# Performance work log

Hardware: AMD Instinct MI355X
Metric: run time of the kernel (lower is better)

The kernel has to match this reference:

```python
import jax, jax.numpy as jnp
import numpy as np

N, E = 50000, 250000
SD, VM = 128, 64          # scalar channels, vector multiplicity (irreps: 128x0e + 64x1e)
EA, SH = 64, 4            # edge_attr dim, spherical-harmonics dim (1x0e + 1x1e)
H, FC = 16, 256
HD = FC // H              # head dim = 16
EPS = 1e-5


def _split(x):
    return x[:, :SD], x[:, SD:].reshape(-1, VM, 3)


def _ln(s, V):
    # equivariant layer norm: standardize scalars; RMS-normalize vector norms
    s = (s - s.mean(-1, keepdims=True)) * jax.lax.rsqrt(s.var(-1, keepdims=True) + EPS)
    vn = jax.lax.rsqrt(jnp.mean(jnp.sum(V * V, -1), -1, keepdims=True) + EPS)
    return s, V * vn[..., None]


def setup_inputs() -> dict:
    key = jax.random.key(0)
    ks = iter(jax.random.split(key, 48))
    rn = lambda shp, sc=1.0: jax.random.normal(next(ks), shp, dtype=jnp.float32) * sc
    w = lambda i, o: rn((i, o), 1.0 / np.sqrt(i))
    z = lambda d: jnp.zeros((d,), jnp.float32)
    return dict(
        node_features=rn((N, SD + 3 * VM)),
        edge_attr=rn((E, EA)),
        edge_sh=rn((E, SH)),
        Wq=w(SD, FC), bq=z(FC),
        Wk=w(SD, FC), bk=z(FC),
        We=w(EA, FC), be=z(FC),
        Wv_s=w(SD, SD), bv_s=z(SD), Wv_v=w(VM, VM),
        w_ss=w(SD, SD), w_vv_s=w(VM, SD), w_ssg=w(SD, VM), w_vvg=w(VM, VM),
        b_ms=z(SD), b_mg=z(VM),
        w_sv=w(SD, VM), w_vs=w(VM, VM), w_vvv=w(VM, VM),
        Wo_s=w(SD, SD), bo_s=z(SD), Wo_v=w(VM, VM),
        W1_s=w(SD, SD + VM), b1_s=z(SD + VM), W1_v=w(VM, VM),
        W2_s=w(SD, SD), b2_s=z(SD), W2_v=w(VM, VM),
        edge_index=jax.random.randint(next(ks), (2, E), 0, N, dtype=jnp.int32),
        batch=jnp.zeros((N,), jnp.int32),
    )


def reference(node_features, edge_attr, edge_sh, Wq, bq, Wk, bk, We, be,
              Wv_s, bv_s, Wv_v, w_ss, w_vv_s, w_ssg, w_vvg, b_ms, b_mg,
              w_sv, w_vs, w_vvv, Wo_s, bo_s, Wo_v,
              W1_s, b1_s, W1_v, W2_s, b2_s, W2_v, edge_index, batch):
    src, dst = edge_index[0], edge_index[1]
    ns, nV = _split(node_features)                        # [N,SD], [N,VM,3]

    # per-edge multi-head attention scores (gathered q/k + edge bias term)
    q = (ns[dst] @ Wq + bq).reshape(-1, H, HD)
    k = (ns[src] @ Wk + bk).reshape(-1, H, HD)
    ef = (edge_attr @ We + be).reshape(-1, H, HD)
    scores = ((q * k).sum(-1) + (q * ef).sum(-1)) / np.sqrt(HD)   # [E,H]

    # per-destination-node softmax (replaces the python unique(dst) loop)
    m = jax.ops.segment_max(scores, dst, num_segments=N)
    ex = jnp.exp(scores - m[dst])
    den = jax.ops.segment_sum(ex, dst, num_segments=N)
    attn = (ex / den[dst]).mean(-1, keepdims=True)                # [E,1]

    # v projection (o3.Linear) on source nodes
    vs = ns[src] @ Wv_s + bv_s                                    # [E,SD]
    Vv = jnp.einsum('evk,vu->euk', nV[src], Wv_v)                 # [E,VM,3]

    # message MLP: fully-connected tensor product with edge SH, norm, swish-gate
    shs, shv = edge_sh[:, 0], edge_sh[:, 1:4]
    s_in = vs * shs[:, None]                                      # 0e x 0e -> 0e
    dots = jnp.einsum('evk,ek->ev', Vv, shv)                      # 1e x 1e -> 0e
    ms = s_in @ w_ss + dots @ w_vv_s + b_ms                       # [E,SD] scalars
    mg = s_in @ w_ssg + dots @ w_vvg + b_mg                       # [E,VM] gates
    MV = ((vs @ w_sv)[:, :, None] * shv[:, None, :]               # 0e x 1e -> 1e
          + jnp.einsum('evk,vu->euk', Vv * shs[:, None, None], w_vs)   # 1e x 0e -> 1e
          + jnp.einsum('evk,vu->euk', jnp.cross(Vv, shv[:, None, :]), w_vvv))  # 1e x 1e -> 1e
    sg, MVn = _ln(jnp.concatenate([ms, mg], -1), MV)
    msg_s = jax.nn.silu(sg[:, :SD])
    msg_V = MVn * jax.nn.sigmoid(sg[:, SD:])[:, :, None]

    # attention-weighted scatter-sum aggregation to destination nodes
    agg_s = jax.ops.segment_sum(msg_s * attn, dst, num_segments=N)
    agg_V = jax.ops.segment_sum(msg_V * attn[:, :, None], dst, num_segments=N)

    # out projection + residual + norm1
    x_s = ns + (agg_s @ Wo_s + bo_s)
    x_V = nV + jnp.einsum('nvk,vu->nuk', agg_V, Wo_v)
    x_s, x_V = _ln(x_s, x_V)

    # gated equivariant FFN + residual + norm2
    f = x_s @ W1_s + b1_s                                         # [N,SD+VM]
    fV = jnp.einsum('nvk,vu->nuk', x_V, W1_v)
    gV = fV * jax.nn.sigmoid(f[:, SD:])[:, :, None]
    o_s = x_s + (jax.nn.silu(f[:, :SD]) @ W2_s + b2_s)
    o_V = x_V + jnp.einsum('nvk,vu->nuk', gV, W2_v)
    o_s, o_V = _ln(o_s, o_V)
    return jnp.concatenate([o_s, o_V.reshape(-1, 3 * VM)], -1)
```

## Files before the change

### kernel.cpp

```cpp
#include <hip/hip_runtime.h>
#include <hip/hip_bf16.h>

#define NNODE 50000
#define NEDGE 250000

typedef __hip_bfloat16 bf16;
typedef __attribute__((ext_vector_type(8))) short short8v;
typedef __attribute__((ext_vector_type(4))) float f32x4;

__device__ __forceinline__ float b2f(bf16 x){ return __bfloat162float(x); }
__device__ __forceinline__ bf16  f2b(float x){ return __float2bfloat16(x); }
__device__ __forceinline__ short f2s(float x){ bf16 h=f2b(x); short s; __builtin_memcpy(&s,&h,2); return s; }
__device__ __forceinline__ float s2f(short s){ bf16 h; __builtin_memcpy(&h,&s,2); return b2f(h); }
__device__ __forceinline__ float sigm(float x){ return 1.0f/(1.0f+__expf(-x)); }
__device__ __forceinline__ float wred64(float v){
  #pragma unroll
  for(int o=32;o>0;o>>=1) v+=__shfl_xor(v,o,64);
  return v;
}
__device__ __forceinline__ float gred16(float v){
  v+=__shfl_xor(v,1,64); v+=__shfl_xor(v,2,64); v+=__shfl_xor(v,4,64); v+=__shfl_xor(v,8,64);
  return v;
}
__device__ __forceinline__ int ired64(int v){
  #pragma unroll
  for(int o=32;o>0;o>>=1) v+=__shfl_xor(v,o,64);
  return v;
}
__device__ __forceinline__ int fragOff(int r, int k){
  int kt=k>>5, k32=k&31, half=k32>>4, g=(k32&15)>>2, j=k32&3;
  return (kt<<10)+((r+(g<<4))<<4)+(half<<3)+(j<<1);
}
__device__ __forceinline__ short8v pack8(float4 a, float4 b){
  short8v s; s[0]=f2s(a.x);s[1]=f2s(a.y);s[2]=f2s(a.z);s[3]=f2s(a.w);
  s[4]=f2s(b.x);s[5]=f2s(b.y);s[6]=f2s(b.z);s[7]=f2s(b.w); return s;
}
__device__ __forceinline__ short8v pack8s(short4 a, short4 b){
  short8v s; s[0]=a.x;s[1]=a.y;s[2]=a.z;s[3]=a.w;s[4]=b.x;s[5]=b.y;s[6]=b.z;s[7]=b.w; return s;
}

#define T_WOS 0
#define T_WOV 32
#define T_W1S 40
#define T_W1V 88
#define T_W2S 96
#define T_W2V 128
#define T_WE  136
#define T_WQ  168
#define T_WK  232
#define T_WVS 296
#define T_WSS 328
#define T_WSSG 360
#define T_WSV 376
#define T_WVV 392
#define T_WVVS 400
#define T_WVVG 416
#define T_WVS2 424
#define T_WVVV 432
#define T_TOT 440

__global__ __launch_bounds__(64) void k_prep(
  const float* __restrict__ Wo_s, const float* __restrict__ Wo_v,
  const float* __restrict__ W1_s, const float* __restrict__ W1_v,
  const float* __restrict__ W2_s, const float* __restrict__ W2_v,
  const float* __restrict__ WeM,
  const float* __restrict__ Wq, const float* __restrict__ Wk,
  const float* __restrict__ Wv_s,
  const float* __restrict__ w_ss, const float* __restrict__ w_ssg,
  const float* __restrict__ w_sv,
  const float* __restrict__ Wv_v, const float* __restrict__ w_vv_s,
  const float* __restrict__ w_vvg, const float* __restrict__ w_vs,
  const float* __restrict__ w_vvv,
  short* __restrict__ P)
{
  const int T=blockIdx.x, l=threadIdx.x;
  const float* W; int N, KT, lt;
  if(T<T_WOV){ W=Wo_s; N=128; KT=4; lt=T; }
  else if(T<T_W1S){ W=Wo_v; N=64; KT=2; lt=T-T_WOV; }
  else if(T<T_W1V){ W=W1_s; N=192; KT=4; lt=T-T_W1S; }
  else if(T<T_W2S){ W=W1_v; N=64; KT=2; lt=T-T_W1V; }
  else if(T<T_W2V){ W=W2_s; N=128; KT=4; lt=T-T_W2S; }
  else if(T<T_WE){ W=W2_v; N=64; KT=2; lt=T-T_W2V; }
  else if(T<T_WQ){ W=WeM; N=256; KT=2; lt=T-T_WE; }
  else if(T<T_WK){ W=Wq; N=256; KT=4; lt=T-T_WQ; }
  else if(T<T_WVS){ W=Wk; N=256; KT=4; lt=T-T_WK; }
  else if(T<T_WSS){ W=Wv_s; N=128; KT=4; lt=T-T_WVS; }
  else if(T<T_WSSG){ W=w_ss; N=128; KT=4; lt=T-T_WSS; }
  else if(T<T_WSV){ W=w_ssg; N=64; KT=4; lt=T-T_WSSG; }
  else if(T<T_WVV){ W=w_sv; N=64; KT=4; lt=T-T_WSV; }
  else if(T<T_WVVS){ W=Wv_v; N=64; KT=2; lt=T-T_WVV; }
  else if(T<T_WVVG){ W=w_vv_s; N=128; KT=2; lt=T-T_WVVS; }
  else if(T<T_WVS2){ W=w_vvg; N=64; KT=2; lt=T-T_WVVG; }
  else if(T<T_WVVV){ W=w_vs; N=64; KT=2; lt=T-T_WVS2; }
  else { W=w_vvv; N=64; KT=2; lt=T-T_WVVV; }
  const int nt=lt/KT, kt=lt-nt*KT;
  const int col=nt*16+(l&15);
  short8v o;
  #pragma unroll
  for(int j=0;j<8;j++){
    int k=kt*32+((j>>2)<<4)+((l>>4)<<2)+(j&3);
    o[j]=f2s(W[(size_t)k*N+col]);
  }
  *(short8v*)(P+((size_t)T<<9)+(l<<3))=o;
}


__global__ __launch_bounds__(256) void k1_mfma(
  const float* __restrict__ nf, const short* __restrict__ P,
  const float* __restrict__ bq, const float* __restrict__ bk,
  const float* __restrict__ bvs,
  bf16* __restrict__ Q, bf16* __restrict__ K, short* __restrict__ NREC2)
{
  __shared__ __align__(16) short nsF[4*512];
  __shared__ __align__(16) short vsF[4*512];
  const int t=threadIdx.x, l=t&63, w=t>>6;
  const int n0=blockIdx.x*16;
  for(int i=t;i<512;i+=256){
    int r=i>>5, c=(i&31)<<2;
    const float4 v=*(const float4*)&nf[(size_t)(n0+r)*320+c];
    short4 s; s.x=f2s(v.x); s.y=f2s(v.y); s.z=f2s(v.z); s.w=f2s(v.w);
    *(short4*)((char*)nsF+fragOff(r,c))=s;
  }
  __syncthreads();
  short8v a[4];
  #pragma unroll
  for(int kt=0;kt<4;kt++) a[kt]=*(const short8v*)((const char*)nsF+(kt<<10)+(l<<4));
  #pragma unroll
  for(int ii=0;ii<4;ii++){
    int nt=w+(ii<<2);
    f32x4 accq={0.f,0.f,0.f,0.f}, acck={0.f,0.f,0.f,0.f};
    #pragma unroll
    for(int kt=0;kt<4;kt++){
      short8v bq8=*(const short8v*)(P+(((size_t)(T_WQ+nt*4+kt))<<9)+(l<<3));
      short8v bk8=*(const short8v*)(P+(((size_t)(T_WK+nt*4+kt))<<9)+(l<<3));
      accq=__builtin_amdgcn_mfma_f32_16x16x32_bf16(a[kt],bq8,accq,0,0,0);
      acck=__builtin_amdgcn_mfma_f32_16x16x32_bf16(a[kt],bk8,acck,0,0,0);
    }
    int col=(nt<<4)+(l&15);
    float bqs=bq[col], bks=bk[col];
    #pragma unroll
    for(int r=0;r<4;r++){
      int row=((l>>4)<<2)+r;
      Q[(size_t)(n0+row)*256+col]=f2b(accq[r]+bqs);
      K[(size_t)(n0+row)*256+col]=f2b(acck[r]+bks);
    }
  }
  #pragma unroll
  for(int ii=0;ii<2;ii++){
    int nt=w+(ii<<2);
    f32x4 acc={0.f,0.f,0.f,0.f};
    #pragma unroll
    for(int kt=0;kt<4;kt++){
      short8v b=*(const short8v*)(P+(((size_t)(T_WVS+nt*4+kt))<<9)+(l<<3));
      acc=__builtin_amdgcn_mfma_f32_16x16x32_bf16(a[kt],b,acc,0,0,0);
    }
    int col=(nt<<4)+(l&15);
    float bv=bvs[col];
    #pragma unroll
    for(int r=0;r<4;r++){
      int row=((l>>4)<<2)+r;
      *(short*)((char*)vsF+fragOff(row,col))=f2s(acc[r]+bv);
    }
  }
  __syncthreads();
  #pragma unroll
  for(int kt=0;kt<4;kt++) a[kt]=*(const short8v*)((const char*)vsF+(kt<<10)+(l<<4));
  #pragma unroll
  for(int ii=0;ii<4;ii++){
    int nt=w+(ii<<2);
    int bt;
    if(nt<8) bt=T_WSS+nt*4;
    else if(nt<12) bt=T_WSSG+(nt-8)*4;
    else bt=T_WSV+(nt-12)*4;
    f32x4 acc={0.f,0.f,0.f,0.f};
    #pragma unroll
    for(int kt=0;kt<4;kt++){
      short8v b=*(const short8v*)(P+(((size_t)(bt+kt))<<9)+(l<<3));
      acc=__builtin_amdgcn_mfma_f32_16x16x32_bf16(a[kt],b,acc,0,0,0);
    }
    int col=(nt<<4)+(l&15);
    int lane, sslot;
    if(nt<8){ lane=col&63; sslot=(col>=64)?1:0; }
    else if(nt<12){ lane=col-128; sslot=2; }
    else { lane=col-192; sslot=3; }
    #pragma unroll
    for(int r=0;r<4;r++){
      int row=((l>>4)<<2)+r;
      NREC2[(size_t)(n0+row)*1280 + (lane<<2) + sslot]=f2s(acc[r]);
    }
  }
}

__global__ __launch_bounds__(256) void k2_mfma(
  const float* __restrict__ nf, const short* __restrict__ P,
  short* __restrict__ NREC2)
{
  __shared__ __align__(16) short nvF[6*512];
  __shared__ __align__(16) short vvF[6*512];
  const int t=threadIdx.x, l=t&63, w=t>>6;
  const int n0=blockIdx.x*16;
  for(int i=t;i<3072;i+=256){
    int r=i/192, c=i-r*192;
    int v=c/3, k=c-3*v;
    float x=nf[(size_t)(n0+r)*320+128+c];
    *(short*)((char*)nvF+(k<<11)+fragOff(r,v))=f2s(x);
  }
  __syncthreads();
  #pragma unroll
  for(int jj=0;jj<3;jj++){
    int job=w+(jj<<2);
    int p=job>>2, nt=job&3;
    f32x4 acc={0.f,0.f,0.f,0.f};
    #pragma unroll
    for(int kt=0;kt<2;kt++){
      short8v a2=*(const short8v*)((const char*)nvF+(p<<11)+(kt<<10)+(l<<4));
      short8v b=*(const short8v*)(P+(((size_t)(T_WVV+nt*2+kt))<<9)+(l<<3));
      acc=__builtin_amdgcn_mfma_f32_16x16x32_bf16(a2,b,acc,0,0,0);
    }
    int col=(nt<<4)+(l&15);
    #pragma unroll
    for(int r=0;r<4;r++){
      int row=((l>>4)<<2)+r;
      *(short*)((char*)vvF+(p<<11)+fragOff(row,col))=f2s(acc[r]);
    }
  }
  __syncthreads();
  #pragma unroll
  for(int jj=0;jj<15;jj++){
    int job=w+(jj<<2);
    int p=job/20, r20=job-p*20;
    int nt, bt, G0;
    if(r20<8){ nt=r20; bt=T_WVVS+nt*2; G0=0; }
    else if(r20<12){ nt=r20-8; bt=T_WVVG+nt*2; G0=1; }
    else if(r20<16){ nt=r20-12; bt=T_WVS2+nt*2; G0=2; }
    else { nt=r20-16; bt=T_WVVV+nt*2; G0=3; }
    f32x4 acc={0.f,0.f,0.f,0.f};
    #pragma unroll
    for(int kt=0;kt<2;kt++){
      short8v a2=*(const short8v*)((const char*)vvF+(p<<11)+(kt<<10)+(l<<4));
      short8v b=*(const short8v*)(P+(((size_t)(bt+kt))<<9)+(l<<3));
      acc=__builtin_amdgcn_mfma_f32_16x16x32_bf16(a2,b,acc,0,0,0);
    }
    int col=(nt<<4)+(l&15);
    int G;
    if(G0==0)      G = p*2 + (col>=64 ? 1 : 0);
    else if(G0==1) G = 6 + p;
    else if(G0==2) G = 9 + p;
    else           G = 12 + p;
    int lane = col & 63;
    int addr = ((1+(G>>2))<<8) + (lane<<2) + (G&3);
    #pragma unroll
    for(int r=0;r<4;r++){
      int row=((l>>4)<<2)+r;
      NREC2[(size_t)(n0+row)*1280 + addr]=f2s(acc[r]);
    }
  }
}

#define SCAN_NB 196

__global__ __launch_bounds__(256) void k_scan1(const int* __restrict__ counts, int* __restrict__ bsum){
  const int t=threadIdx.x, ln=t&63, wid=t>>6;
  int idx=blockIdx.x*256+t;
  int v=(idx<NNODE)?counts[idx]:0;
  int s=ired64(v);
  __shared__ int ws[4];
  if(ln==0) ws[wid]=s;
  __syncthreads();
  if(t==0) bsum[blockIdx.x]=ws[0]+ws[1]+ws[2]+ws[3];
}

__global__ __launch_bounds__(256) void k_scan2(const int* __restrict__ bsum, int* __restrict__ boff){
  const int t=threadIdx.x, ln=t&63, wid=t>>6;
  int v=(t<SCAN_NB)?bsum[t]:0;
  int incl=v;
  #pragma unroll
  for(int o=1;o<64;o<<=1){ int x=__shfl_up(incl,o,64); if(ln>=o) incl+=x; }
  __shared__ int wtot[4], wpre[4];
  if(ln==63) wtot[wid]=incl;
  __syncthreads();
  if(t==0){ int s=0; for(int k=0;k<4;k++){ wpre[k]=s; s+=wtot[k]; } }
  __syncthreads();
  if(t<SCAN_NB) boff[t]=wpre[wid]+incl-v;
}

__global__ __launch_bounds__(256) void k_scan3(const int* __restrict__ counts, const int* __restrict__ boff,
                                               int* __restrict__ off, int* __restrict__ cursor){
  const int t=threadIdx.x, ln=t&63, wid=t>>6;
  int idx=blockIdx.x*256+t;
  int v=(idx<NNODE)?counts[idx]:0;
  int incl=v;
  #pragma unroll
  for(int o=1;o<64;o<<=1){ int x=__shfl_up(incl,o,64); if(ln>=o) incl+=x; }
  __shared__ int wtot[4], wpre[4];
  if(ln==63) wtot[wid]=incl;
  __syncthreads();
  if(t==0){ int s=0; for(int k=0;k<4;k++){ wpre[k]=s; s+=wtot[k]; } }
  __syncthreads();
  int excl=boff[blockIdx.x]+wpre[wid]+incl-v;
  if(idx<NNODE){ off[idx]=excl; cursor[idx]=excl; }
  if(idx==NNODE) off[NNODE]=NEDGE;
  if(blockIdx.x==SCAN_NB-1 && t==255) off[NNODE]=NEDGE;
}

__global__ __launch_bounds__(256) void k_scatter(
  const int* __restrict__ eidx, const float* __restrict__ esh,
  int* __restrict__ cursor, int* __restrict__ eord,
  int* __restrict__ srcs, float* __restrict__ eshs)
{
  int e=blockIdx.x*256+threadIdx.x;
  if(e<NEDGE){
    int d=eidx[NEDGE+e];
    int pos=atomicAdd(&cursor[d],1);
    eord[pos]=e;
    srcs[pos]=eidx[e];
    *(float4*)&eshs[(size_t)pos*4]=*(const float4*)&esh[(size_t)e*4];
  }
}

__global__ __launch_bounds__(256) void k3_mfma(
  const float* __restrict__ eattr, const int* __restrict__ eidx,
  const short* __restrict__ P, const float* __restrict__ be,
  const bf16* __restrict__ Q, const bf16* __restrict__ K,
  float* __restrict__ SC, int* __restrict__ counts)
{
  __shared__ __align__(16) short aeF[2*512];
  __shared__ __align__(16) float ef[16][260];
  __shared__ int ssrc[16], sdst[16];
  const int t=threadIdx.x, l=t&63, w=t>>6;
  const int e0=blockIdx.x*16;
  if(t<16){
    ssrc[t]=eidx[e0+t];
    int d=eidx[NEDGE+e0+t];
    sdst[t]=d;
    atomicAdd(&counts[d],1);
  }
  {
    int r=t>>4, c4=(t&15)<<2;
    const float4 v=*(const float4*)&eattr[(size_t)(e0+r)*64+c4];
    short4 s; s.x=f2s(v.x); s.y=f2s(v.y); s.z=f2s(v.z); s.w=f2s(v.w);
    *(short4*)((char*)aeF+fragOff(r,c4))=s;
  }
  __syncthreads();
  {
    short8v a0=*(const short8v*)((const char*)aeF+(l<<4));
    short8v a1=*(const short8v*)((const char*)aeF+1024+(l<<4));
    #pragma unroll
    for(int ii=0;ii<4;ii++){
      int nt=w+(ii<<2);
      f32x4 acc={0.f,0.f,0.f,0.f};
      short8v b0=*(const short8v*)(P+(((size_t)(T_WE+nt*2+0))<<9)+(l<<3));
      short8v b1=*(const short8v*)(P+(((size_t)(T_WE+nt*2+1))<<9)+(l<<3));
      acc=__builtin_amdgcn_mfma_f32_16x16x32_bf16(a0,b0,acc,0,0,0);
      acc=__builtin_amdgcn_mfma_f32_16x16x32_bf16(a1,b1,acc,0,0,0);
      int col=(nt<<4)+(l&15);
      float bv=be[col];
      #pragma unroll
      for(int r=0;r<4;r++){ int row=((l>>4)<<2)+r; ef[row][col]=acc[r]+bv; }
    }
  }
  __syncthreads();
  {
    const int h=l&15, qt=l>>4;
    const int ch=h*16+(qt<<2);
    #pragma unroll
    for(int j=0;j<4;j++){
      int el=w*4+j;
      int s=ssrc[el], d=sdst[el];
      short4 qs=*(const short4*)((const short*)Q+(size_t)d*256+ch);
      short4 ks=*(const short4*)((const short*)K+(size_t)s*256+ch);
      const float4 e4=*(const float4*)&ef[el][ch];
      float p = s2f(qs.x)*(s2f(ks.x)+e4.x)
              + s2f(qs.y)*(s2f(ks.y)+e4.y)
              + s2f(qs.z)*(s2f(ks.z)+e4.z)
              + s2f(qs.w)*(s2f(ks.w)+e4.w);
      p += __shfl_xor(p,16,64);
      p += __shfl_xor(p,32,64);
      if(qt==0) SC[(size_t)(e0+el)*16+h]=p*0.25f;
    }
  }
}

__global__ __launch_bounds__(256) void k5_att(
  const float* __restrict__ SC, const int* __restrict__ OFF,
  const int* __restrict__ EORD, float* __restrict__ ATTs)
{
  const int l=threadIdx.x&63;
  const int n=blockIdx.x*4+(threadIdx.x>>6);
  const int beg=OFF[n], end=OFF[n+1];
  const int j=l>>4, h=l&15;
  float mh=-1e30f;
  for(int i=beg+j;i<end;i+=4) mh=fmaxf(mh, SC[(size_t)EORD[i]*16+h]);
  mh=fmaxf(mh,__shfl_xor(mh,16,64));
  mh=fmaxf(mh,__shfl_xor(mh,32,64));
  float dh=0.f;
  for(int i=beg+j;i<end;i+=4) dh+=__expf(SC[(size_t)EORD[i]*16+h]-mh);
  dh+=__shfl_xor(dh,16,64);
  dh+=__shfl_xor(dh,32,64);
  float rdh=(end>beg)?1.f/dh:0.f;
  for(int i0=beg;i0<end;i0+=4){
    int i=i0+j;
    float a=0.f; bool act=(i<end);
    if(act) a=__expf(SC[(size_t)EORD[i]*16+h]-mh)*rdh;
    a=gred16(a);
    if(h==0 && act) ATTs[i]=a*(1.f/16.f);
  }
}

__global__ __launch_bounds__(256) void k6_agg(
  const int* __restrict__ SRCs, const float* __restrict__ ESHs,
  const short* __restrict__ NREC2, const float* __restrict__ ATTs,
  const int* __restrict__ OFF,
  const float* __restrict__ b_ms, const float* __restrict__ b_mg,
  float* __restrict__ AGS, float* __restrict__ AGV)
{
  const int l = threadIdx.x & 63;
  const int n = blockIdx.x*4 + (threadIdx.x>>6);
  const int beg=OFF[n], end=OFF[n+1];
  const float bmsa=b_ms[l], bmsb=b_ms[64+l], bmgv=b_mg[l];

  float as0=0.f,as1=0.f,av0acc=0.f,av1acc=0.f,av2acc=0.f;
  for(int i=beg;i<end;i++){
    const int s=SRCs[i];
    const float att=ATTs[i];
    const float4 sh4=*(const float4*)&ESHs[(size_t)i*4];
    const float shs=sh4.x, sh0=sh4.y, sh1=sh4.z, sh2=sh4.w;

    const short* R = NREC2 + (size_t)s*1280 + (l<<2);
    const short4 q0=*(const short4*)(R);
    const short4 q1=*(const short4*)(R+256);
    const short4 q2=*(const short4*)(R+512);
    const short4 q3=*(const short4*)(R+768);
    const short4 q4=*(const short4*)(R+1024);

    float msa = shs*s2f(q0.x) + s2f(q1.x)*sh0 + s2f(q1.z)*sh1 + s2f(q2.x)*sh2 + bmsa;
    float msb = shs*s2f(q0.y) + s2f(q1.y)*sh0 + s2f(q1.w)*sh1 + s2f(q2.y)*sh2 + bmsb;
    float mgv = shs*s2f(q0.z) + s2f(q2.z)*sh0 + s2f(q2.w)*sh1 + s2f(q3.x)*sh2 + bmgv;

    float sum = wred64(msa+msb+mgv);
    float sq  = wred64(msa*msa+msb*msb+mgv*mgv);
    float mean = sum*(1.f/192.f);
    float var  = sq*(1.f/192.f) - mean*mean;
    float rs   = rsqrtf(var + 1e-5f);

    const float svv=s2f(q0.w);
    const float w0=s2f(q3.y), w1=s2f(q3.z), w2=s2f(q3.w);
    const float c0=s2f(q4.x), c1=s2f(q4.y), c2=s2f(q4.z);
    float cr0 = c1*sh2 - c2*sh1;
    float cr1 = c2*sh0 - c0*sh2;
    float cr2 = c0*sh1 - c1*sh0;
    float mv0 = svv*sh0 + shs*w0 + cr0;
    float mv1 = svv*sh1 + shs*w1 + cr1;
    float mv2 = svv*sh2 + shs*w2 + cr2;
    float vsq = wred64(mv0*mv0+mv1*mv1+mv2*mv2);
    float vn  = rsqrtf(vsq*(1.f/64.f) + 1e-5f);

    float sga=(msa-mean)*rs, sgb=(msb-mean)*rs, sgg=(mgv-mean)*rs;
    float wV = vn * sigm(sgg) * att;
    as0 += sga*sigm(sga)*att;
    as1 += sgb*sigm(sgb)*att;
    av0acc += mv0*wV;
    av1acc += mv1*wV;
    av2acc += mv2*wV;
  }
  AGS[(size_t)n*128+l]     =as0;
  AGS[(size_t)n*128+64+l]  =as1;
  AGV[(size_t)n*192+l]     =av0acc;
  AGV[(size_t)n*192+64+l]  =av1acc;
  AGV[(size_t)n*192+128+l] =av2acc;
}

__global__ __launch_bounds__(256) void k7_mfma(
  const float* __restrict__ nf,
  const float* __restrict__ AGS, const float* __restrict__ AGV,
  const short* __restrict__ P,
  const float* __restrict__ bo_s, const float* __restrict__ b1_s, const float* __restrict__ b2_s,
  float* __restrict__ out)
{
  __shared__ float xs[16][132];
  __shared__ float xv[16][196];
  __shared__ short ffh[16][204];
  __shared__ __align__(16) short asA[4*512];
  __shared__ __align__(16) short avA[6*512];
  __shared__ float smean[16], srs[16], svn[16];
  const int t=threadIdx.x, l=t&63, w=t>>6;
  const int n0=blockIdx.x*16;
  const int lam=t&63, kt4=t>>6;
  const int fr=lam&15, fg=lam>>4;

  for(int i=t;i<2048;i+=256){ int r=i>>7,c=i&127; xs[r][c]=nf[(size_t)(n0+r)*320+c]; }
  for(int i=t;i<3072;i+=256){ int r=i/192,cc=i-r*192; int k=cc>>6,u=cc&63; xv[r][cc]=nf[(size_t)(n0+r)*320+128+u*3+k]; }
  {
    const float* base=&AGS[(size_t)(n0+fr)*128 + (kt4<<5) + (fg<<2)];
    float4 va=*(const float4*)base, vb=*(const float4*)(base+16);
    *(short8v*)((char*)asA+(kt4<<10)+(lam<<4))=pack8(va,vb);
  }
  for(int i=t;i<384;i+=256){
    int seg=i>>6, lm=i&63, r=lm&15, g=lm>>4;
    int p=seg>>1, k2=seg&1;
    const float* base=&AGV[(size_t)(n0+r)*192 + (p<<6) + (k2<<5) + (g<<2)];
    float4 va=*(const float4*)base, vb=*(const float4*)(base+16);
    *(short8v*)((char*)avA+(seg<<10)+(lm<<4))=pack8(va,vb);
  }
  __syncthreads();

  {
    short8v a[4];
    #pragma unroll
    for(int kt=0;kt<4;kt++) a[kt]=*(const short8v*)((const char*)asA+(kt<<10)+(l<<4));
    #pragma unroll
    for(int ii=0;ii<2;ii++){
      int nt=w+(ii<<2);
      f32x4 acc={0.f,0.f,0.f,0.f};
      #pragma unroll
      for(int kt=0;kt<4;kt++){
        short8v b=*(const short8v*)(P+(((size_t)(T_WOS+nt*4+kt))<<9)+(l<<3));
        acc=__builtin_amdgcn_mfma_f32_16x16x32_bf16(a[kt],b,acc,0,0,0);
      }
      int col=(nt<<4)+(l&15);
      float bv=bo_s[col];
      #pragma unroll
      for(int r=0;r<4;r++){ int row=((l>>4)<<2)+r; xs[row][col]+=acc[r]+bv; }
    }
    #pragma unroll
    for(int ii=0;ii<3;ii++){
      int tid=w*3+ii, p=tid>>2, nt2=tid&3;
      f32x4 acc={0.f,0.f,0.f,0.f};
      #pragma unroll
      for(int kt=0;kt<2;kt++){
        short8v a2=*(const short8v*)((const char*)avA+(((p<<1)+kt)<<10)+(l<<4));
        short8v b=*(const short8v*)(P+(((size_t)(T_WOV+nt2*2+kt))<<9)+(l<<3));
        acc=__builtin_amdgcn_mfma_f32_16x16x32_bf16(a2,b,acc,0,0,0);
      }
      int col=(p<<6)+(nt2<<4)+(l&15);
      #pragma unroll
      for(int r=0;r<4;r++){ int row=((l>>4)<<2)+r; xv[row][col]+=acc[r]; }
    }
  }
  __syncthreads();

  {
    const int nn=t>>4, g=t&15;
    float sum=0,sq=0;
    #pragma unroll
    for(int j=0;j<8;j++){ float x=xs[nn][g+16*j]; sum+=x; sq+=x*x; }
    sum=gred16(sum); sq=gred16(sq);
    float mean=sum*(1.f/128.f);
    float var=sq*(1.f/128.f)-mean*mean;
    float vsq=0;
    #pragma unroll
    for(int j=0;j<12;j++){ float x=xv[nn][g+16*j]; vsq+=x*x; }
    vsq=gred16(vsq);
    if(g==0){ smean[nn]=mean; srs[nn]=rsqrtf(var+1e-5f); svn[nn]=rsqrtf(vsq*(1.f/64.f)+1e-5f); }
  }
  __syncthreads();

  for(int i=t;i<512;i+=256){
    int r=i>>5, c=(i&31)<<2;
    float m=smean[r], rs=srs[r];
    float4 v=*(float4*)&xs[r][c];
    v.x=(v.x-m)*rs; v.y=(v.y-m)*rs; v.z=(v.z-m)*rs; v.w=(v.w-m)*rs;
    *(float4*)&xs[r][c]=v;
  }
  for(int i=t;i<768;i+=256){
    int r=i/48, c=(i-r*48)<<2;
    float vn=svn[r];
    float4 v=*(float4*)&xv[r][c];
    v.x*=vn; v.y*=vn; v.z*=vn; v.w*=vn;
    *(float4*)&xv[r][c]=v;
  }
  __syncthreads();
  {
    float4 va=*(const float4*)&xs[fr][(kt4<<5)+(fg<<2)];
    float4 vb=*(const float4*)&xs[fr][(kt4<<5)+16+(fg<<2)];
    *(short8v*)((char*)asA+(kt4<<10)+(lam<<4))=pack8(va,vb);
  }
  for(int i=t;i<384;i+=256){
    int seg=i>>6, lm=i&63, r=lm&15, g=lm>>4;
    int p=seg>>1, k2=seg&1;
    float4 va=*(const float4*)&xv[r][(p<<6)+(k2<<5)+(g<<2)];
    float4 vb=*(const float4*)&xv[r][(p<<6)+(k2<<5)+16+(g<<2)];
    *(short8v*)((char*)avA+(seg<<10)+(lm<<4))=pack8(va,vb);
  }
  __syncthreads();

  {
    short8v a[4];
    #pragma unroll
    for(int kt=0;kt<4;kt++) a[kt]=*(const short8v*)((const char*)asA+(kt<<10)+(l<<4));
    #pragma unroll
    for(int ii=0;ii<3;ii++){
      int nt=w+(ii<<2);
      f32x4 acc={0.f,0.f,0.f,0.f};
      #pragma unroll
      for(int kt=0;kt<4;kt++){
        short8v b=*(const short8v*)(P+(((size_t)(T_W1S+nt*4+kt))<<9)+(l<<3));
        acc=__builtin_amdgcn_mfma_f32_16x16x32_bf16(a[kt],b,acc,0,0,0);
      }
      int col=(nt<<4)+(l&15);
      float bv=b1_s[col];
      #pragma unroll
      for(int r=0;r<4;r++){ int row=((l>>4)<<2)+r; ffh[row][col]=f2s(acc[r]+bv); }
    }
  }
  __syncthreads();

  f32x4 g4acc[3];
  {
    #pragma unroll
    for(int ii=0;ii<3;ii++){
      int tid=w*3+ii, p=tid>>2, nt2=tid&3;
      f32x4 acc={0.f,0.f,0.f,0.f};
      #pragma unroll
      for(int kt=0;kt<2;kt++){
        short8v a2=*(const short8v*)((const char*)avA+(((p<<1)+kt)<<10)+(l<<4));
        short8v b=*(const short8v*)(P+(((size_t)(T_W1V+nt2*2+kt))<<9)+(l<<3));
        acc=__builtin_amdgcn_mfma_f32_16x16x32_bf16(a2,b,acc,0,0,0);
      }
      g4acc[ii]=acc;
    }
    for(int i=t;i<512;i+=256){
      int r=i>>5, c=(i&31)<<2;
      short4 sv4=*(short4*)&ffh[r][c];
      float x0=s2f(sv4.x), x1=s2f(sv4.y), x2=s2f(sv4.z), x3=s2f(sv4.w);
      sv4.x=f2s(x0*sigm(x0)); sv4.y=f2s(x1*sigm(x1)); sv4.z=f2s(x2*sigm(x2)); sv4.w=f2s(x3*sigm(x3));
      *(short4*)&ffh[r][c]=sv4;
    }
  }
  __syncthreads();

  {
    short4 sa=*(const short4*)&ffh[fr][(kt4<<5)+(fg<<2)];
    short4 sb=*(const short4*)&ffh[fr][(kt4<<5)+16+(fg<<2)];
    *(short8v*)((char*)asA+(kt4<<10)+(lam<<4))=pack8s(sa,sb);
  }
  {
    #pragma unroll
    for(int ii=0;ii<3;ii++){
      int tid=w*3+ii, nt2=tid&3;
      int uu=(nt2<<4)+(l&15);
      #pragma unroll
      for(int r=0;r<4;r++){
        int row=((l>>4)<<2)+r;
        g4acc[ii][r]*=sigm(s2f(ffh[row][128+uu]));
      }
    }
  }
  __syncthreads();

  {
    #pragma unroll
    for(int ii=0;ii<3;ii++){
      int tid=w*3+ii, p=tid>>2, nt2=tid&3;
      int uu=(nt2<<4)+(l&15);
      #pragma unroll
      for(int r=0;r<4;r++){
        int row=((l>>4)<<2)+r;
        ffh[row][(p<<6)+uu]=f2s(g4acc[ii][r]);
      }
    }
  }
  __syncthreads();
  for(int i=t;i<384;i+=256){
    int seg=i>>6, lm=i&63, r=lm&15, g=lm>>4;
    int p=seg>>1, k2=seg&1;
    short4 sa=*(const short4*)&ffh[r][(p<<6)+(k2<<5)+(g<<2)];
    short4 sb=*(const short4*)&ffh[r][(p<<6)+(k2<<5)+16+(g<<2)];
    *(short8v*)((char*)avA+(seg<<10)+(lm<<4))=pack8s(sa,sb);
  }
  __syncthreads();

  {
    short8v a[4];
    #pragma unroll
    for(int kt=0;kt<4;kt++) a[kt]=*(const short8v*)((const char*)asA+(kt<<10)+(l<<4));
    #pragma unroll
    for(int ii=0;ii<2;ii++){
      int nt=w+(ii<<2);
      f32x4 acc={0.f,0.f,0.f,0.f};
      #pragma unroll
      for(int kt=0;kt<4;kt++){
        short8v b=*(const short8v*)(P+(((size_t)(T_W2S+nt*4+kt))<<9)+(l<<3));
        acc=__builtin_amdgcn_mfma_f32_16x16x32_bf16(a[kt],b,acc,0,0,0);
      }
      int col=(nt<<4)+(l&15);
      float bv=b2_s[col];
      #pragma unroll
      for(int r=0;r<4;r++){ int row=((l>>4)<<2)+r; xs[row][col]+=acc[r]+bv; }
    }
    #pragma unroll
    for(int ii=0;ii<3;ii++){
      int tid=w*3+ii, p=tid>>2, nt2=tid&3;
      f32x4 acc={0.f,0.f,0.f,0.f};
      #pragma unroll
      for(int kt=0;kt<2;kt++){
        short8v a2=*(const short8v*)((const char*)avA+(((p<<1)+kt)<<10)+(l<<4));
        short8v b=*(const short8v*)(P+(((size_t)(T_W2V+nt2*2+kt))<<9)+(l<<3));
        acc=__builtin_amdgcn_mfma_f32_16x16x32_bf16(a2,b,acc,0,0,0);
      }
      int col=(p<<6)+(nt2<<4)+(l&15);
      #pragma unroll
      for(int r=0;r<4;r++){ int row=((l>>4)<<2)+r; xv[row][col]+=acc[r]; }
    }
  }
  __syncthreads();

  {
    const int nn=t>>4, g=t&15;
    float sum=0,sq=0;
    #pragma unroll
    for(int j=0;j<8;j++){ float x=xs[nn][g+16*j]; sum+=x; sq+=x*x; }
    sum=gred16(sum); sq=gred16(sq);
    float mean=sum*(1.f/128.f);
    float var=sq*(1.f/128.f)-mean*mean;
    float vsq=0;
    #pragma unroll
    for(int j=0;j<12;j++){ float x=xv[nn][g+16*j]; vsq+=x*x; }
    vsq=gred16(vsq);
    if(g==0){ smean[nn]=mean; srs[nn]=rsqrtf(var+1e-5f); svn[nn]=rsqrtf(vsq*(1.f/64.f)+1e-5f); }
  }
  __syncthreads();

  for(int i=t;i<16*320;i+=256){
    int nn=i/320, c=i-nn*320;
    float v;
    if(c<128) v=(xs[nn][c]-smean[nn])*srs[nn];
    else { int j=c-128; int u=j/3, k=j-u*3; v=xv[nn][(k<<6)+u]*svn[nn]; }
    out[(size_t)(n0+nn)*320+c]=v;
  }
}

extern "C" void kernel_launch(void* const* d_in, const int* in_sizes, int n_in,
                              void* d_out, int out_size, void* d_ws, size_t ws_size,
                              hipStream_t stream)
{
  (void)in_sizes; (void)n_in; (void)out_size; (void)ws_size;
  const float* nf    =(const float*)d_in[0];
  const float* eattr =(const float*)d_in[1];
  const float* esh   =(const float*)d_in[2];
  const float* Wq    =(const float*)d_in[3];  const float* bq  =(const float*)d_in[4];
  const float* Wk    =(const float*)d_in[5];  const float* bk  =(const float*)d_in[6];
  const float* We    =(const float*)d_in[7];  const float* be  =(const float*)d_in[8];
  const float* Wv_s  =(const float*)d_in[9];  const float* bv_s=(const float*)d_in[10];
  const float* Wv_v  =(const float*)d_in[11];
  const float* w_ss  =(const float*)d_in[12]; const float* w_vv_s=(const float*)d_in[13];
  const float* w_ssg =(const float*)d_in[14]; const float* w_vvg =(const float*)d_in[15];
  const float* b_ms  =(const float*)d_in[16]; const float* b_mg  =(const float*)d_in[17];
  const float* w_sv  =(const float*)d_in[18]; const float* w_vs  =(const float*)d_in[19];
  const float* w_vvv =(const float*)d_in[20];
  const float* Wo_s  =(const float*)d_in[21]; const float* bo_s  =(const float*)d_in[22];
  const float* Wo_v  =(const float*)d_in[23];
  const float* W1_s  =(const float*)d_in[24]; const float* b1_s  =(const float*)d_in[25];
  const float* W1_v  =(const float*)d_in[26];
  const float* W2_s  =(const float*)d_in[27]; const float* b2_s  =(const float*)d_in[28];
  const float* W2_v  =(const float*)d_in[29];
  const int*   eidx  =(const int*)d_in[30];
  float* out=(float*)d_out;

  char* w=(char*)d_ws;
  bf16* Q    =(bf16*)w;  w+=(size_t)NNODE*256*2;
  bf16* Kb   =(bf16*)w;  w+=(size_t)NNODE*256*2;
  short* NREC2=(short*)w; w+=(size_t)NNODE*1280*2;
  float* SC  =(float*)w; w+=(size_t)NEDGE*16*4;
  float* ESHs=(float*)w; w+=(size_t)NEDGE*4*4;
  float* ATTs=(float*)w; w+=(size_t)NEDGE*4;
  float* AGS =(float*)w; w+=(size_t)NNODE*128*4;
  float* AGV =(float*)w; w+=(size_t)NNODE*192*4;
  short* P   =(short*)w; w+=(size_t)T_TOT*512*2;
  int* COUNTS=(int*)w;   w+=(size_t)NNODE*4;
  int* OFFb  =(int*)w;   w+=(size_t)(NNODE+1)*4;
  int* CURSOR=(int*)w;   w+=(size_t)NNODE*4;
  int* EORDb =(int*)w;   w+=(size_t)NEDGE*4;
  int* SRCs  =(int*)w;   w+=(size_t)NEDGE*4;
  int* BSUM  =(int*)w;   w+=(size_t)256*4;
  int* BOFF  =(int*)w;   w+=(size_t)256*4;

  hipMemsetAsync(COUNTS,0,(size_t)NNODE*4,stream);

  k_prep    <<<T_TOT,64,0,stream>>>(Wo_s,Wo_v,W1_s,W1_v,W2_s,W2_v,We,
                                    Wq,Wk,Wv_s,w_ss,w_ssg,w_sv,
                                    Wv_v,w_vv_s,w_vvg,w_vs,w_vvv,P);
  k1_mfma   <<<NNODE/16,256,0,stream>>>(nf,P,bq,bk,bv_s,Q,Kb,NREC2);
  k2_mfma   <<<NNODE/16,256,0,stream>>>(nf,P,NREC2);
  k3_mfma   <<<NEDGE/16,256,0,stream>>>(eattr,eidx,P,be,Q,Kb,SC,COUNTS);
  k_scan1   <<<SCAN_NB,256,0,stream>>>(COUNTS,BSUM);
  k_scan2   <<<1,256,0,stream>>>(BSUM,BOFF);
  k_scan3   <<<SCAN_NB,256,0,stream>>>(COUNTS,BOFF,OFFb,CURSOR);
  k_scatter <<<(NEDGE+255)/256,256,0,stream>>>(eidx,esh,CURSOR,EORDb,SRCs,ESHs);
  k5_att    <<<NNODE/4,256,0,stream>>>(SC,OFFb,EORDb,ATTs);
  k6_agg    <<<NNODE/4,256,0,stream>>>(SRCs,ESHs,NREC2,ATTs,OFFb,b_ms,b_mg,AGS,AGV);
  k7_mfma   <<<NNODE/16,256,0,stream>>>(nf,AGS,AGV,P,bo_s,b1_s,b2_s,out);
}
```

Before: 459.6 us.

## Precompute per-node quadratic moments to replace per-edge wave reductions in aggregation

Adds a per-node kernel that reduces the source-node record into sums, cross-products and Gram-like moments. The aggregation kernel can then compute the per-edge layer-norm mean, variance and vector RMS in closed form from the edge spherical harmonics, without three 64-lane shuffle reductions per edge. This trades an extra kernel pass over the node records, plus a 128-byte per-source read per edge, for fewer cross-lane operations in the edge loop. It also changes rounding, because variance is now formed from expanded quadratic forms, which risks cancellation.

```diff
diff --git a/kernel.cpp b/kernel.cpp
--- a/kernel.cpp
+++ b/kernel.cpp
@@ -257,6 +257,70 @@
   }
 }
 
+__global__ __launch_bounds__(256) void k4_stats(
+  const short* __restrict__ NREC2,
+  const float* __restrict__ b_ms, const float* __restrict__ b_mg,
+  float* __restrict__ SREC)
+{
+  const int l=threadIdx.x&63;
+  const int n=blockIdx.x*4+(threadIdx.x>>6);
+  const float b1=b_ms[l], b2=b_ms[64+l], b3=b_mg[l];
+  const short* R=NREC2+(size_t)n*1280+(l<<2);
+  const short4 q0=*(const short4*)(R);
+  const short4 q1=*(const short4*)(R+256);
+  const short4 q2=*(const short4*)(R+512);
+  const short4 q3=*(const short4*)(R+768);
+  const short4 q4=*(const short4*)(R+1024);
+  const float a1=s2f(q0.x), a2=s2f(q0.y), a3=s2f(q0.z), sv=s2f(q0.w);
+  const float d1x=s2f(q1.x), d1y=s2f(q1.z), d1z=s2f(q2.x);
+  const float d2x=s2f(q1.y), d2y=s2f(q1.w), d2z=s2f(q2.y);
+  const float d3x=s2f(q2.z), d3y=s2f(q2.w), d3z=s2f(q3.x);
+  const float Wx=s2f(q3.y), Wy=s2f(q3.z), Wz=s2f(q3.w);
+  const float Cx=s2f(q4.x), Cy=s2f(q4.y), Cz=s2f(q4.z);
+
+  float sA  = wred64(a1+a2+a3);
+  float sDx = wred64(d1x+d2x+d3x);
+  float sDy = wred64(d1y+d2y+d3y);
+  float sDz = wred64(d1z+d2z+d3z);
+  float qAA = wred64(a1*a1+a2*a2+a3*a3);
+  float qADx= wred64(a1*d1x+a2*d2x+a3*d3x);
+  float qADy= wred64(a1*d1y+a2*d2y+a3*d3y);
+  float qADz= wred64(a1*d1z+a2*d2z+a3*d3z);
+  float qDDxx=wred64(d1x*d1x+d2x*d2x+d3x*d3x);
+  float qDDyy=wred64(d1y*d1y+d2y*d2y+d3y*d3y);
+  float qDDzz=wred64(d1z*d1z+d2z*d2z+d3z*d3z);
+  float qDDxy=wred64(d1x*d1y+d2x*d2y+d3x*d3y);
+  float qDDxz=wred64(d1x*d1z+d2x*d2z+d3x*d3z);
+  float qDDyz=wred64(d1y*d1z+d2y*d2z+d3y*d3z);
+  float qAb = wred64(a1*b1+a2*b2+a3*b3);
+  float qDbx= wred64(b1*d1x+b2*d2x+b3*d3x);
+  float qDby= wred64(b1*d1y+b2*d2y+b3*d3y);
+  float qDbz= wred64(b1*d1z+b2*d2z+b3*d3z);
+  float vC1 = wred64(sv*sv + Cx*Cx+Cy*Cy+Cz*Cz);
+  float vCCxx=wred64(Cx*Cx);
+  float vCCyy=wred64(Cy*Cy);
+  float vCCzz=wred64(Cz*Cz);
+  float vCCxy=wred64(Cx*Cy);
+  float vCCxz=wred64(Cx*Cz);
+  float vCCyz=wred64(Cy*Cz);
+  float vWW = wred64(Wx*Wx+Wy*Wy+Wz*Wz);
+  float vSWCx=wred64(sv*Wx + (Wy*Cz-Wz*Cy));
+  float vSWCy=wred64(sv*Wy + (Wz*Cx-Wx*Cz));
+  float vSWCz=wred64(sv*Wz + (Wx*Cy-Wy*Cx));
+
+  if(l==0){
+    float4* O=(float4*)(SREC+(size_t)n*32);
+    O[0]=make_float4(sA,sDx,sDy,sDz);
+    O[1]=make_float4(qAA,qADx,qADy,qADz);
+    O[2]=make_float4(qDDxx,qDDyy,qDDzz,qDDxy);
+    O[3]=make_float4(qDDxz,qDDyz,qAb,0.f);
+    O[4]=make_float4(qDbx,qDby,qDbz,vC1);
+    O[5]=make_float4(vCCxx,vCCyy,vCCzz,vCCxy);
+    O[6]=make_float4(vCCxz,vCCyz,vWW,0.f);
+    O[7]=make_float4(vSWCx,vSWCy,vSWCz,0.f);
+  }
+}
+
 #define SCAN_NB 196
 
 __global__ __launch_bounds__(256) void k_scan1(const int* __restrict__ counts, int* __restrict__ bsum){
@@ -299,7 +363,6 @@
   __syncthreads();
   int excl=boff[blockIdx.x]+wpre[wid]+incl-v;
   if(idx<NNODE){ off[idx]=excl; cursor[idx]=excl; }
-  if(idx==NNODE) off[NNODE]=NEDGE;
   if(blockIdx.x==SCAN_NB-1 && t==255) off[NNODE]=NEDGE;
 }
 
@@ -410,7 +473,7 @@
 __global__ __launch_bounds__(256) void k6_agg(
   const int* __restrict__ SRCs, const float* __restrict__ ESHs,
   const short* __restrict__ NREC2, const float* __restrict__ ATTs,
-  const int* __restrict__ OFF,
+  const float* __restrict__ SREC, const int* __restrict__ OFF,
   const float* __restrict__ b_ms, const float* __restrict__ b_mg,
   float* __restrict__ AGS, float* __restrict__ AGV)
 {
@@ -418,6 +481,8 @@
   const int n = blockIdx.x*4 + (threadIdx.x>>6);
   const int beg=OFF[n], end=OFF[n+1];
   const float bmsa=b_ms[l], bmsb=b_ms[64+l], bmgv=b_mg[l];
+  const float cb1 = wred64(bmsa+bmsb+bmgv);
+  const float cb2 = wred64(bmsa*bmsa+bmsb*bmsb+bmgv*bmgv);
 
   float as0=0.f,as1=0.f,av0acc=0.f,av1acc=0.f,av2acc=0.f;
   for(int i=beg;i<end;i++){
@@ -426,6 +491,16 @@
     const float4 sh4=*(const float4*)&ESHs[(size_t)i*4];
     const float shs=sh4.x, sh0=sh4.y, sh1=sh4.z, sh2=sh4.w;
 
+    const float* SR = SREC + (size_t)s*32;
+    const float4 F0=*(const float4*)(SR);
+    const float4 F1=*(const float4*)(SR+4);
+    const float4 F2=*(const float4*)(SR+8);
+    const float4 F3=*(const float4*)(SR+12);
+    const float4 F4=*(const float4*)(SR+16);
+    const float4 F5=*(const float4*)(SR+20);
+    const float4 F6=*(const float4*)(SR+24);
+    const float4 F7=*(const float4*)(SR+28);
+
     const short* R = NREC2 + (size_t)s*1280 + (l<<2);
     const short4 q0=*(const short4*)(R);
     const short4 q1=*(const short4*)(R+256);
@@ -433,15 +508,27 @@
     const short4 q3=*(const short4*)(R+768);
     const short4 q4=*(const short4*)(R+1024);
 
+    const float sum = shs*F0.x + sh0*F0.y + sh1*F0.z + sh2*F0.w + cb1;
+    const float sq  = shs*shs*F1.x
+                    + 2.f*shs*(sh0*F1.y + sh1*F1.z + sh2*F1.w)
+                    + sh0*sh0*F2.x + sh1*sh1*F2.y + sh2*sh2*F2.z
+                    + 2.f*(sh0*sh1*F2.w + sh0*sh2*F3.x + sh1*sh2*F3.y)
+                    + 2.f*shs*F3.z
+                    + 2.f*(sh0*F4.x + sh1*F4.y + sh2*F4.z) + cb2;
+    const float shn2 = sh0*sh0+sh1*sh1+sh2*sh2;
+    const float vsq = shn2*F4.w
+                    - (sh0*sh0*F5.x + sh1*sh1*F5.y + sh2*sh2*F5.z
+                       + 2.f*(sh0*sh1*F5.w + sh0*sh2*F6.x + sh1*sh2*F6.y))
+                    + shs*shs*F6.z
+                    + 2.f*shs*(sh0*F7.x + sh1*F7.y + sh2*F7.z);
+    const float mean = sum*(1.f/192.f);
+    const float var  = sq*(1.f/192.f) - mean*mean;
+    const float rs   = rsqrtf(var + 1e-5f);
+    const float vn   = rsqrtf(vsq*(1.f/64.f) + 1e-5f);
+
     float msa = shs*s2f(q0.x) + s2f(q1.x)*sh0 + s2f(q1.z)*sh1 + s2f(q2.x)*sh2 + bmsa;
     float msb = shs*s2f(q0.y) + s2f(q1.y)*sh0 + s2f(q1.w)*sh1 + s2f(q2.y)*sh2 + bmsb;
     float mgv = shs*s2f(q0.z) + s2f(q2.z)*sh0 + s2f(q2.w)*sh1 + s2f(q3.x)*sh2 + bmgv;
-
-    float sum = wred64(msa+msb+mgv);
-    float sq  = wred64(msa*msa+msb*msb+mgv*mgv);
-    float mean = sum*(1.f/192.f);
-    float var  = sq*(1.f/192.f) - mean*mean;
-    float rs   = rsqrtf(var + 1e-5f);
 
     const float svv=s2f(q0.w);
     const float w0=s2f(q3.y), w1=s2f(q3.z), w2=s2f(q3.w);
@@ -452,8 +539,6 @@
     float mv0 = svv*sh0 + shs*w0 + cr0;
     float mv1 = svv*sh1 + shs*w1 + cr1;
     float mv2 = svv*sh2 + shs*w2 + cr2;
-    float vsq = wred64(mv0*mv0+mv1*mv1+mv2*mv2);
-    float vn  = rsqrtf(vsq*(1.f/64.f) + 1e-5f);
 
     float sga=(msa-mean)*rs, sgb=(msb-mean)*rs, sgg=(mgv-mean)*rs;
     float wV = vn * sigm(sgg) * att;
@@ -774,6 +859,7 @@
   int* SRCs  =(int*)w;   w+=(size_t)NEDGE*4;
   int* BSUM  =(int*)w;   w+=(size_t)256*4;
   int* BOFF  =(int*)w;   w+=(size_t)256*4;
+  float* SREC=(float*)Q;
 
   hipMemsetAsync(COUNTS,0,(size_t)NNODE*4,stream);
 
@@ -783,11 +869,12 @@
   k1_mfma   <<<NNODE/16,256,0,stream>>>(nf,P,bq,bk,bv_s,Q,Kb,NREC2);
   k2_mfma   <<<NNODE/16,256,0,stream>>>(nf,P,NREC2);
   k3_mfma   <<<NEDGE/16,256,0,stream>>>(eattr,eidx,P,be,Q,Kb,SC,COUNTS);
+  k4_stats  <<<NNODE/4,256,0,stream>>>(NREC2,b_ms,b_mg,SREC);
   k_scan1   <<<SCAN_NB,256,0,stream>>>(COUNTS,BSUM);
   k_scan2   <<<1,256,0,stream>>>(BSUM,BOFF);
   k_scan3   <<<SCAN_NB,256,0,stream>>>(COUNTS,BOFF,OFFb,CURSOR);
   k_scatter <<<(NEDGE+255)/256,256,0,stream>>>(eidx,esh,CURSOR,EORDb,SRCs,ESHs);
   k5_att    <<<NNODE/4,256,0,stream>>>(SC,OFFb,EORDb,ATTs);
-  k6_agg    <<<NNODE/4,256,0,stream>>>(SRCs,ESHs,NREC2,ATTs,OFFb,b_ms,b_mg,AGS,AGV);
+  k6_agg    <<<NNODE/4,256,0,stream>>>(SRCs,ESHs,NREC2,ATTs,SREC,OFFb,b_ms,b_mg,AGS,AGV);
   k7_mfma   <<<NNODE/16,256,0,stream>>>(nf,AGS,AGV,P,bo_s,b1_s,b2_s,out);
 }
```

After: 579.3 us. 26.0% more time.
